# Optimization experiments

Hardware: AMD Instinct MI355X
Metric: run time of the kernel (lower is better)

## Reference

```python
import jax, jax.numpy as jnp
import numpy as np

L = 2
S = (L + 1) ** 2            # 9 spherical harmonic coefficients
C = 128                     # sphere_channels
H = 128                     # hidden_channels
NH = 8                      # num_heads
A = 32                      # attn_alpha_channels
V = 16                      # attn_value_channels
N = 5000                    # nodes
E = 50000                   # edges
DE = 128                    # invariant edge embedding dim
G = 18                      # S2 grid points

# l of each coefficient in l-major layout [S]
L_OF = np.concatenate([np.full(2 * l + 1, l) for l in range(L + 1)])
IDX_M0 = np.array([l * l + l for l in range(L + 1)])

def _idx_m(m):
    neg = np.array([l * l + l - m for l in range(m, L + 1)])
    pos = np.array([l * l + l + m for l in range(m, L + 1)])
    return neg, pos

IDX_M1_NEG, IDX_M1_POS = _idx_m(1)
IDX_M2_NEG, IDX_M2_POS = _idx_m(2)
# m-major ordering and its inverse permutation back to l-major
PERM = np.concatenate([IDX_M0, IDX_M1_POS, IDX_M1_NEG, IDX_M2_POS, IDX_M2_NEG])
INV_PERM = np.argsort(PERM)


def _silu(x):
    return x * jax.nn.sigmoid(x)


def _layernorm(x, g, b, eps=1e-5):
    mu = x.mean(-1, keepdims=True)
    var = ((x - mu) ** 2).mean(-1, keepdims=True)
    return (x - mu) * jax.lax.rsqrt(var + eps) * g + b


def _smooth_leaky_relu(x, a=0.2):
    return 0.5 * (1 + a) * x + 0.5 * (1 - a) * x * (2 * jax.nn.sigmoid(x) - 1)


def _so2_conv(x, w_m0, b_m0, w_m1, w_m2, cout):
    """SO(2) convolution on rotated embeddings. x: [E,S,Cin] l-major.
    Returns ([E,S,cout] l-major, extra m=0 channels)."""
    e = x.shape[0]
    # m = 0: plain linear over flattened (L+1)*Cin
    x0 = x[:, IDX_M0, :].reshape(e, -1)
    y0 = x0 @ w_m0 + b_m0
    y0_main = y0[:, : (L + 1) * cout].reshape(e, L + 1, cout)
    y0_extra = y0[:, (L + 1) * cout:]
    parts = [y0_main]
    # m > 0: complex (cos/sin) SO2 mixing with shared weight for real/imag
    for neg, pos, w in ((IDX_M1_NEG, IDX_M1_POS, w_m1), (IDX_M2_NEG, IDX_M2_POS, w_m2)):
        nl = len(neg)
        xr = x[:, pos, :].reshape(e, -1)
        xi = x[:, neg, :].reshape(e, -1)
        yr = xr @ w  # [E, 2*nl*cout]
        yi = xi @ w
        yr_r, yr_i = yr[:, : nl * cout], yr[:, nl * cout:]
        yi_r, yi_i = yi[:, : nl * cout], yi[:, nl * cout:]
        parts.append((yr_r - yi_i).reshape(e, nl, cout))   # +m (real)
        parts.append((yr_i + yi_r).reshape(e, nl, cout))   # -m (imag)
    out_m = jnp.concatenate(parts, axis=1)                 # m-major
    return out_m[:, INV_PERM, :], y0_extra


def _s2_act(x, togrid, fromgrid):
    g = jnp.einsum('gs,esc->egc', togrid, x)
    return jnp.einsum('sg,egc->esc', fromgrid, _silu(g))


def _sep_s2_act(scalars, x, togrid, fromgrid):
    t = _s2_act(x, togrid, fromgrid)
    return jnp.concatenate([_silu(scalars)[:, None, :], t[:, 1:, :]], axis=1)


def _so3_linear(x, w, b):
    # w: [L+1, Cin, Cout], shared across m within each l; bias only on l=0
    out = jnp.einsum('nsc,sco->nso', x, w[L_OF])
    return out.at[:, 0, :].add(b)


def _eqv_norm(x, g, b, eps=1e-5):
    # l=0: layernorm over channels; l>0: RMS over (m, channels) per degree
    outs = [_layernorm(x[:, 0:1, :], g[0], b)]
    for l in range(1, L + 1):
        sl = x[:, l * l:(l + 1) * (l + 1), :]
        rms = jnp.sqrt(jnp.mean(sl ** 2, axis=(1, 2), keepdims=True) + eps)
        outs.append(sl / rms * g[l])
    return jnp.concatenate(outs, axis=1)


def _forward(x, edge_distance, wigner, rad_w1, rad_b1, rad_ln_g, rad_ln_b, rad_w2, rad_b2,
             w1_m0, b1_m0, w1_m1, w1_m2, w2_m0, b2_m0, w2_m1, w2_m2,
             alpha_ln_g, alpha_ln_b, alpha_dot, proj_w, proj_b,
             norm1_g, norm1_b, norm2_g, norm2_b,
             gate_w, gate_b, ffn_w1, ffn_b1, ffn_w2, ffn_b2,
             togrid, fromgrid, edge_src, edge_dst):
    # ---------- SO2 equivariant graph attention ----------
    xn = _eqv_norm(x, norm1_g, norm1_b)
    msg = jnp.concatenate([xn[edge_src], xn[edge_dst]], axis=-1)      # [E,S,2C]
    msg = jnp.einsum('eij,ejc->eic', wigner, msg)                     # rotate to edge frame
    # radial function shared across m within each l (use_m_share_rad)
    h = _silu(_layernorm(edge_distance @ rad_w1 + rad_b1, rad_ln_g, rad_ln_b))
    rad = (h @ rad_w2 + rad_b2).reshape(-1, L + 1, 2 * C)             # [E,L+1,2C]
    msg = msg * rad[:, L_OF, :]
    hid, x0_extra = _so2_conv(msg, w1_m0, b1_m0, w1_m1, w1_m2, H)
    x_alpha = x0_extra[:, : NH * A].reshape(-1, NH, A)
    gating = x0_extra[:, NH * A:]                                     # [E,H]
    hid = _sep_s2_act(gating, hid, togrid, fromgrid)
    val, _ = _so2_conv(hid, w2_m0, b2_m0, w2_m1, w2_m2, NH * V)
    val = jnp.einsum('eji,ejc->eic', wigner, val)                     # rotate back (D^T)
    # attention weights with per-destination segment softmax
    a = _smooth_leaky_relu(_layernorm(x_alpha, alpha_ln_g, alpha_ln_b))
    a = jnp.einsum('eha,ha->eh', a, alpha_dot)                        # [E,NH]
    amax = jax.ops.segment_max(a, edge_dst, num_segments=N)
    aexp = jnp.exp(a - amax[edge_dst])
    asum = jax.ops.segment_sum(aexp, edge_dst, num_segments=N)
    attn = aexp / asum[edge_dst]
    msg_out = (val.reshape(-1, S, NH, V) * attn[:, None, :, None]).reshape(-1, S, NH * V)
    node = jax.ops.segment_sum(msg_out, edge_dst, num_segments=N)     # [N,S,NH*V]
    x = x + _so3_linear(node, proj_w, proj_b)
    # ---------- spherical FFN (sep S2 gating) ----------
    xn = _eqv_norm(x, norm2_g, norm2_b)
    gating = xn[:, 0, :] @ gate_w + gate_b
    hh = _so3_linear(xn, ffn_w1, ffn_b1)
    hh = _sep_s2_act(gating, hh, togrid, fromgrid)
    return x + _so3_linear(hh, ffn_w2, ffn_b2)


def setup_inputs() -> dict:
    key = jax.random.key(0)
    ks = iter(jax.random.split(key, 64))
    def nrm(shape, scale=1.0):
        return jax.random.normal(next(ks), shape, dtype=jnp.float32) * scale
    EX = NH * A + H
    inp = {}
    inp['x'] = nrm((N, S, C))
    inp['edge_distance'] = nrm((E, DE))
    inp['wigner'] = nrm((E, S, S), 1.0 / np.sqrt(S))
    inp['rad_w1'] = nrm((DE, 64), 1.0 / np.sqrt(DE)); inp['rad_b1'] = jnp.zeros((64,), jnp.float32)
    inp['rad_ln_g'] = jnp.ones((64,), jnp.float32); inp['rad_ln_b'] = jnp.zeros((64,), jnp.float32)
    inp['rad_w2'] = nrm((64, 2 * C * (L + 1)), 0.05); inp['rad_b2'] = jnp.ones((2 * C * (L + 1),), jnp.float32)
    inp['w1_m0'] = nrm(((L + 1) * 2 * C, (L + 1) * H + EX), 1.0 / np.sqrt((L + 1) * 2 * C))
    inp['b1_m0'] = jnp.zeros(((L + 1) * H + EX,), jnp.float32)
    inp['w1_m1'] = nrm((2 * 2 * C, 2 * 2 * H), 1.0 / np.sqrt(2 * 2 * C))
    inp['w1_m2'] = nrm((2 * C, 2 * H), 1.0 / np.sqrt(2 * C))
    inp['w2_m0'] = nrm(((L + 1) * H, (L + 1) * NH * V), 1.0 / np.sqrt((L + 1) * H))
    inp['b2_m0'] = jnp.zeros(((L + 1) * NH * V,), jnp.float32)
    inp['w2_m1'] = nrm((2 * H, 2 * 2 * NH * V), 1.0 / np.sqrt(2 * H))
    inp['w2_m2'] = nrm((H, 2 * NH * V), 1.0 / np.sqrt(H))
    inp['alpha_ln_g'] = jnp.ones((A,), jnp.float32); inp['alpha_ln_b'] = jnp.zeros((A,), jnp.float32)
    inp['alpha_dot'] = nrm((NH, A), 1.0 / np.sqrt(A))
    inp['proj_w'] = nrm((L + 1, NH * V, C), 1.0 / np.sqrt(NH * V)); inp['proj_b'] = jnp.zeros((C,), jnp.float32)
    inp['norm1_g'] = jnp.ones((L + 1, C), jnp.float32); inp['norm1_b'] = jnp.zeros((C,), jnp.float32)
    inp['norm2_g'] = jnp.ones((L + 1, C), jnp.float32); inp['norm2_b'] = jnp.zeros((C,), jnp.float32)
    inp['gate_w'] = nrm((C, H), 1.0 / np.sqrt(C)); inp['gate_b'] = jnp.zeros((H,), jnp.float32)
    inp['ffn_w1'] = nrm((L + 1, C, H), 1.0 / np.sqrt(C)); inp['ffn_b1'] = jnp.zeros((H,), jnp.float32)
    inp['ffn_w2'] = nrm((L + 1, H, C), 1.0 / np.sqrt(H)); inp['ffn_b2'] = jnp.zeros((C,), jnp.float32)
    inp['togrid'] = nrm((G, S), 1.0 / np.sqrt(S))
    inp['fromgrid'] = nrm((S, G), 1.0 / np.sqrt(G))
    inp['edge_src'] = jax.random.randint(next(ks), (E,), 0, N)
    inp['edge_dst'] = jax.random.randint(next(ks), (E,), 0, N)
    return inp


def reference(x, edge_distance, wigner, rad_w1, rad_b1, rad_ln_g, rad_ln_b, rad_w2, rad_b2,
              w1_m0, b1_m0, w1_m1, w1_m2, w2_m0, b2_m0, w2_m1, w2_m2,
              alpha_ln_g, alpha_ln_b, alpha_dot, proj_w, proj_b,
              norm1_g, norm1_b, norm2_g, norm2_b,
              gate_w, gate_b, ffn_w1, ffn_b1, ffn_w2, ffn_b2,
              togrid, fromgrid, edge_src, edge_dst):
    return _forward(x, edge_distance, wigner, rad_w1, rad_b1, rad_ln_g, rad_ln_b, rad_w2, rad_b2,
                    w1_m0, b1_m0, w1_m1, w1_m2, w2_m0, b2_m0, w2_m1, w2_m2,
                    alpha_ln_g, alpha_ln_b, alpha_dot, proj_w, proj_b,
                    norm1_g, norm1_b, norm2_g, norm2_b,
                    gate_w, gate_b, ffn_w1, ffn_b1, ffn_w2, ffn_b2,
                    togrid, fromgrid, edge_src, edge_dst)
```

## Files before the change

kernel.cpp:

```cpp
#include <hip/hip_runtime.h>
#include <hip/hip_bf16.h>

typedef unsigned short u16;
typedef unsigned int   u32;
typedef __attribute__((ext_vector_type(8))) short short8;
typedef __attribute__((ext_vector_type(4))) float float4v;

#define NN 5000
#define EE 50000

__device__ __forceinline__ float b2f(u16 u){ return __uint_as_float(((u32)u)<<16); }
__device__ __forceinline__ u16 f2b(float f){
  u32 x = __float_as_uint(f);
  u32 r = (x + 0x7fffu + ((x>>16)&1u)) >> 16;
  return (u16)r;
}
__device__ __forceinline__ float ldin(const void* p, size_t i, bool f32){
  return f32 ? ((const float*)p)[i] : b2f(((const u16*)p)[i]);
}
__device__ __forceinline__ float siluf(float x){ return x/(1.f+__expf(-x)); }
__device__ __forceinline__ float waveRedSum(float v){
  #pragma unroll
  for (int m=32;m>=1;m>>=1) v += __shfl_xor(v,m,64);
  return v;
}
__device__ __forceinline__ float red32(float v){
  #pragma unroll
  for (int m=16;m>=1;m>>=1) v += __shfl_xor(v,m,64);
  return v;
}


__global__ __launch_bounds__(256) void zero_kernel(float* __restrict__ p, int n){
  for (int i = blockIdx.x*256 + threadIdx.x; i < n; i += gridDim.x*256) p[i] = 0.f;
}

__global__ void detect_kernel(const u32* __restrict__ ng, int* __restrict__ flag){
  if (blockIdx.x == 0 && threadIdx.x == 0) *flag = (ng[0] == 0x3F800000u) ? 1 : 0;
}

__global__ __launch_bounds__(256) void hist_kernel(const int* __restrict__ edst,
    int* __restrict__ counts){
  int e = blockIdx.x*256 + threadIdx.x;
  if (e < EE) atomicAdd(&counts[edst[e]], 1);
}

__global__ __launch_bounds__(1024) void scan_kernel(const int* __restrict__ counts,
    int* __restrict__ row_start, int* __restrict__ cursor){
  __shared__ int buf[1024];
  __shared__ int base;
  const int t = threadIdx.x;
  if (t == 0){ base = 0; row_start[0] = 0; }
  __syncthreads();
  for (int i0 = 0; i0 < NN; i0 += 1024){
    int i = i0 + t;
    int c = (i < NN) ? counts[i] : 0;
    buf[t] = c;
    __syncthreads();
    #pragma unroll
    for (int ofs = 1; ofs < 1024; ofs <<= 1){
      int v = (t >= ofs) ? buf[t-ofs] : 0;
      __syncthreads();
      buf[t] += v;
      __syncthreads();
    }
    if (i < NN){
      int incl = base + buf[t];
      row_start[i+1] = incl;
      cursor[i] = incl - c;
    }
    __syncthreads();
    if (t == 0) base += buf[1023];
    __syncthreads();
  }
}

__global__ __launch_bounds__(256) void place_kernel(const int* __restrict__ edst,
    int* __restrict__ cursor, int* __restrict__ order){
  int e = blockIdx.x*256 + threadIdx.x;
  if (e < EE) order[atomicAdd(&cursor[edst[e]], 1)] = e;
}

__global__ __launch_bounds__(256) void cvt_kernel(const int* __restrict__ dflag,
    const void* __restrict__ src, long long off0, u16* __restrict__ dst, int n){
  const bool f32 = (*dflag != 0);
  for (int i = blockIdx.x*256 + threadIdx.x; i < n; i += gridDim.x*256)
    dst[i] = f32 ? f2b(((const float*)src)[off0 + i]) : ((const u16*)src)[off0 + i];
}

__global__ __launch_bounds__(256) void gathercvt_kernel(const int* __restrict__ dflag,
    const void* __restrict__ src, const int* __restrict__ order, int e0,
    u16* __restrict__ dst, int n){
  const bool f32 = (*dflag != 0);
  for (int i = blockIdx.x*256 + threadIdx.x; i < n; i += gridDim.x*256){
    int le = i >> 7, c = i & 127;
    int eg = order[e0 + le];
    dst[i] = f2b(ldin(src, (size_t)eg*128 + c, f32));
  }
}

__global__ __launch_bounds__(256) void biasprep_kernel(const int* __restrict__ dflag,
    const void* b1,const void* b2,const void* rb1,const void* rb2,
    const void* pb,const void* gb,const void* f1,const void* f2,
    u16* d_b1,u16* d_b2,u16* d_rb1,u16* d_rb2,u16* d_pb,u16* d_gb,u16* d_f1,u16* d_f2){
  const bool f32 = (*dflag != 0);
  int t = blockIdx.x*256 + threadIdx.x;
  if (t < 768) d_b1[t]  = f2b(ldin(b1, t, f32));
  if (t < 384) d_b2[t]  = f2b(ldin(b2, t, f32));
  if (t < 64)  d_rb1[t] = f2b(ldin(rb1, t, f32));
  if (t < 768) d_rb2[t] = f2b(ldin(rb2, t, f32));
  if (t < 128){
    d_pb[t] = f2b(ldin(pb, t, f32));
    d_gb[t] = f2b(ldin(gb, t, f32));
    d_f1[t] = f2b(ldin(f1, t, f32));
    d_f2[t] = f2b(ldin(f2, t, f32));
  }
}

__global__ __launch_bounds__(256) void cvtT_kernel(const int* __restrict__ dflag,
    const void* __restrict__ src, long long off0, u16* __restrict__ dst, int K, int N){
  const bool f32 = (*dflag != 0);
  int total = K*N;
  for (int i = blockIdx.x*256 + threadIdx.x; i < total; i += gridDim.x*256){
    int n = i / K, k = i % K;
    dst[i] = f2b(ldin(src, (size_t)off0 + (size_t)k*N + n, f32));
  }
}

__global__ __launch_bounds__(256) void cvtT3_kernel(const int* __restrict__ dflag,
    const void* __restrict__ src, u16* __restrict__ dst){
  const bool f32 = (*dflag != 0);
  const long long l = blockIdx.y;
  for (int i = blockIdx.x*256 + threadIdx.x; i < 16384; i += gridDim.x*256){
    int n = i >> 7, k = i & 127;
    dst[l*16384 + i] = f2b(ldin(src, (size_t)l*16384 + (size_t)k*128 + n, f32));
  }
}

__global__ __launch_bounds__(256) void wprepT_kernel(const int* __restrict__ dflag,
    const void* __restrict__ w, u16* __restrict__ wt, int K0, int N0){
  const bool f32 = (*dflag != 0);
  int total = 2*N0*2*K0;
  for (int i = blockIdx.x*blockDim.x + threadIdx.x; i < total; i += gridDim.x*blockDim.x){
    int c = i / (2*K0), r = i % (2*K0);
    float v;
    if (r < K0) v = ldin(w, (size_t)r*2*N0 + c, f32);
    else {
      int rr = r - K0;
      if (c < N0) v = -ldin(w, (size_t)rr*2*N0 + N0 + c, f32);
      else        v =  ldin(w, (size_t)rr*2*N0 + (c - N0), f32);
    }
    wt[i] = f2b(v);
  }
}

__global__ __launch_bounds__(128) void eqvnorm_kernel(const int* __restrict__ dflag,
    const void* __restrict__ x, int in_always_f32,
    const void* __restrict__ g, const void* __restrict__ b,
    void* __restrict__ out, int out_f32){
  const bool f32 = (*dflag != 0);
  const bool inf32 = in_always_f32 || f32;
  const int n = blockIdx.x, t = threadIdx.x;
  __shared__ float red[2];
  float v[9];
  #pragma unroll
  for (int s=0;s<9;s++) v[s] = ldin(x, (size_t)n*1152 + s*128 + t, inf32);

  auto bsum = [&](float val)->float{
    float w = waveRedSum(val);
    __syncthreads();
    if ((t & 63) == 0) red[t>>6] = w;
    __syncthreads();
    return red[0] + red[1];
  };
  auto store = [&](int idx, float val){
    if (out_f32) ((float*)out)[(size_t)n*1152 + idx] = val;
    else         ((u16*) out)[(size_t)n*1152 + idx] = f2b(val);
  };
  float mu  = bsum(v[0]) * (1.f/128.f);
  float d0  = v[0] - mu;
  float var = bsum(d0*d0) * (1.f/128.f);
  store(t, d0 * rsqrtf(var + 1e-5f) * ldin(g, t, f32) + ldin(b, t, f32));
  float ss1 = v[1]*v[1] + v[2]*v[2] + v[3]*v[3];
  float inv1 = rsqrtf(bsum(ss1)*(1.f/384.f) + 1e-5f);
  float g1 = ldin(g, 128 + t, f32);
  #pragma unroll
  for (int s=1;s<=3;s++) store(s*128 + t, v[s]*inv1*g1);
  float ss2 = 0.f;
  #pragma unroll
  for (int s=4;s<9;s++) ss2 += v[s]*v[s];
  float inv2 = rsqrtf(bsum(ss2)*(1.f/640.f) + 1e-5f);
  float g2 = ldin(g, 256 + t, f32);
  #pragma unroll
  for (int s=4;s<9;s++) store(s*128 + t, v[s]*inv2*g2);
}

__global__ __launch_bounds__(256) void gemm_mfma_kernel(
    const u16* __restrict__ A, int lda, int K,
    const u16* __restrict__ Wt, int NOUT,
    const u16* __restrict__ bias,
    u16* __restrict__ out0, int ld0, int coloff0, int split,
    u16* __restrict__ out1, int ld1, int M){
  __shared__ __align__(16) u16 As[2][128][40];
  __shared__ __align__(16) u16 Bs[2][128][40];
  const int t = threadIdx.x;
  const int r0 = blockIdx.x * 128;
  const int n0 = blockIdx.y * 128;
  const int lane = t & 63, wave = t >> 6;
  const int wr = (wave & 1) * 64, wn = (wave >> 1) * 64;
  float4v acc[4][4];
  #pragma unroll
  for (int i=0;i<4;i++)
    #pragma unroll
    for (int j=0;j<4;j++) acc[i][j] = (float4v){0.f,0.f,0.f,0.f};

  const int sr = t >> 2, sc = (t & 3) * 8;
  const int fr = lane & 15, fq = (lane >> 4) * 8;

  const u16* aptr0 = A + (size_t)(r0 + sr)*lda + sc;
  const u16* aptr1 = A + (size_t)(r0 + sr + 64)*lda + sc;
  const bool av0 = (r0 + sr) < M, av1 = (r0 + sr + 64) < M;
  const u16* bptr0 = Wt + (size_t)(n0 + sr)*K + sc;
  const u16* bptr1 = Wt + (size_t)(n0 + sr + 64)*K + sc;
  const bool bv0 = (n0 + sr) < NOUT, bv1 = (n0 + sr + 64) < NOUT;
  const uint4 z4 = make_uint4(0u,0u,0u,0u);

  uint4 ra0 = av0 ? *(const uint4*)(aptr0) : z4;
  uint4 ra1 = av1 ? *(const uint4*)(aptr1) : z4;
  uint4 rb0 = bv0 ? *(const uint4*)(bptr0) : z4;
  uint4 rb1 = bv1 ? *(const uint4*)(bptr1) : z4;

  int buf = 0;
  for (int k0 = 0; k0 < K; k0 += 32){
    *(uint4*)&As[buf][sr   ][sc] = ra0;
    *(uint4*)&As[buf][sr+64][sc] = ra1;
    *(uint4*)&Bs[buf][sr   ][sc] = rb0;
    *(uint4*)&Bs[buf][sr+64][sc] = rb1;
    __syncthreads();
    const int k1 = k0 + 32;
    if (k1 < K){
      ra0 = av0 ? *(const uint4*)(aptr0 + k1) : z4;
      ra1 = av1 ? *(const uint4*)(aptr1 + k1) : z4;
      rb0 = bv0 ? *(const uint4*)(bptr0 + k1) : z4;
      rb1 = bv1 ? *(const uint4*)(bptr1 + k1) : z4;
    }
    short8 af[4], bfv[4];
    #pragma unroll
    for (int i=0;i<4;i++){
      af[i]  = *(const short8*)&As[buf][wr + i*16 + fr][fq];
      bfv[i] = *(const short8*)&Bs[buf][wn + i*16 + fr][fq];
    }
    #pragma unroll
    for (int i=0;i<4;i++)
      #pragma unroll
      for (int j=0;j<4;j++)
        acc[i][j] = __builtin_amdgcn_mfma_f32_16x16x32_bf16(af[i], bfv[j], acc[i][j], 0, 0, 0);
    buf ^= 1;
    __syncthreads();
  }
  const int quad = lane >> 4;
  #pragma unroll
  for (int j=0;j<4;j++){
    int col = n0 + wn + j*16 + fr;
    if (col >= NOUT) continue;
    float bv = bias ? b2f(bias[col]) : 0.f;
    #pragma unroll
    for (int i=0;i<4;i++){
      int rbase = r0 + wr + i*16 + quad*4;
      #pragma unroll
      for (int rg=0; rg<4; rg++){
        int row = rbase + rg;
        if (row >= M) continue;
        float v = acc[i][j][rg] + bv;
        if (col < split) out0[(size_t)row*ld0 + coloff0 + col] = f2b(v);
        else             out1[(size_t)row*ld1 + (col - split)] = f2b(v);
      }
    }
  }
}

__global__ __launch_bounds__(256) void gemm_node_kernel(
    const int* __restrict__ dflag,
    const u16* __restrict__ A,
    const u16* __restrict__ W3t,
    const u16* __restrict__ bias,
    const void* __restrict__ resid, int resid_mode,
    void* __restrict__ out, int out_mode, int gate_out){
  const bool f32 = (*dflag != 0);
  const int l = blockIdx.y;
  const int rpn  = (l==0) ? 1 : ((l==1) ? 3 : 5);
  const int soff = (l==0) ? 0 : ((l==1) ? 1 : 4);
  const int M = NN * rpn;
  const int r0 = blockIdx.x * 128;
  if (r0 >= M) return;
  __shared__ __align__(16) u16 As[128][40];
  __shared__ __align__(16) u16 Bs[128][40];
  const int t = threadIdx.x;
  const int lane = t & 63, wave = t >> 6;
  const int wr = (wave & 1) * 64, wn = (wave >> 1) * 64;
  float4v acc[4][4];
  #pragma unroll
  for (int i=0;i<4;i++)
    #pragma unroll
    for (int j=0;j<4;j++) acc[i][j] = (float4v){0.f,0.f,0.f,0.f};

  const int sr = t >> 2, sc = (t & 3) * 8;
  const int fr = lane & 15, fq = (lane >> 4) * 8;
  size_t abase[2]; bool aval[2];
  #pragma unroll
  for (int s2=0;s2<2;s2++){
    int m = r0 + sr + s2*64;
    aval[s2] = m < M;
    int n = m / rpn, srow = soff + (m % rpn);
    abase[s2] = (size_t)n*1152 + srow*128 + sc;
  }
  const u16* Wl = W3t + (size_t)l*16384;

  #pragma unroll
  for (int k0 = 0; k0 < 128; k0 += 32){
    #pragma unroll
    for (int s2=0;s2<2;s2++){
      int row = sr + s2*64;
      uint4 av = make_uint4(0u,0u,0u,0u);
      if (aval[s2]) av = *(const uint4*)(A + abase[s2] + k0);
      *(uint4*)&As[row][sc] = av;
      uint4 wv = *(const uint4*)(Wl + (size_t)row*128 + k0 + sc);
      *(uint4*)&Bs[row][sc] = wv;
    }
    __syncthreads();
    short8 af[4], bfr[4];
    #pragma unroll
    for (int i=0;i<4;i++){
      af[i]  = *(const short8*)&As[wr + i*16 + fr][fq];
      bfr[i] = *(const short8*)&Bs[wn + i*16 + fr][fq];
    }
    #pragma unroll
    for (int i=0;i<4;i++)
      #pragma unroll
      for (int j=0;j<4;j++)
        acc[i][j] = __builtin_amdgcn_mfma_f32_16x16x32_bf16(af[i], bfr[j], acc[i][j], 0, 0, 0);
    __syncthreads();
  }
  const int quad = lane >> 4;
  #pragma unroll
  for (int j=0;j<4;j++){
    int col = wn + j*16 + fr;
    float bv = (bias && l==0) ? b2f(bias[col]) : 0.f;
    #pragma unroll
    for (int i=0;i<4;i++){
      int rbase = r0 + wr + i*16 + quad*4;
      #pragma unroll
      for (int rg=0; rg<4; rg++){
        int m = rbase + rg;
        if (m >= M) continue;
        int n = m / rpn, srow = soff + (m % rpn);
        size_t na = (size_t)n*1152 + srow*128 + col;
        float v = acc[i][j][rg] + bv;
        if (resid_mode == 1)      v += ((const float*)resid)[na];
        else if (resid_mode == 2) v += ldin(resid, na, f32);
        if (gate_out)            ((u16*)out)[(size_t)n*128 + col] = f2b(v);
        else if (out_mode == 0)  ((u16*)out)[na] = f2b(v);
        else if (out_mode == 1)  ((float*)out)[na] = v;
        else { if (f32) ((float*)out)[na] = v; else ((u16*)out)[na] = f2b(v); }
      }
    }
  }
}

__global__ __launch_bounds__(256) void nodecvt_kernel(const float* __restrict__ node,
    const float* __restrict__ nsum, u16* __restrict__ nodeb){
  for (int i = blockIdx.x*256 + threadIdx.x; i < NN*1152; i += gridDim.x*256){
    int n = i / 1152, c = i & 127, h = c >> 4;
    float ns = nsum[(size_t)n*8 + h];
    float rs = (ns > 0.f) ? 1.f/ns : 0.f;
    nodeb[i] = f2b(node[i] * rs);
  }
}

__global__ __launch_bounds__(128) void node_s2act_kernel(const int* __restrict__ dflag,
    const u16* __restrict__ hh, const u16* __restrict__ gating,
    const void* __restrict__ tg, const void* __restrict__ fg, u16* __restrict__ hh2){
  const bool f32 = (*dflag != 0);
  const int n = blockIdx.x, t = threadIdx.x;
  __shared__ float TG[162], FG[162];
  for (int i=t; i<162; i+=128){ TG[i]=ldin(tg,i,f32); FG[i]=ldin(fg,i,f32); }
  float hv[9];
  #pragma unroll
  for (int s=0;s<9;s++) hv[s] = b2f(hh[(size_t)n*1152 + s*128 + t]);
  __syncthreads();
  float gg[18];
  #pragma unroll
  for (int gi=0;gi<18;gi++){
    float a = 0.f;
    #pragma unroll
    for (int s=0;s<9;s++) a = fmaf(TG[gi*9+s], hv[s], a);
    gg[gi] = siluf(a);
  }
  hh2[(size_t)n*1152 + t] = f2b(siluf(b2f(gating[(size_t)n*128 + t])));
  #pragma unroll
  for (int s=1;s<9;s++){
    float a = 0.f;
    #pragma unroll
    for (int gi=0;gi<18;gi++) a = fmaf(FG[s*18+gi], gg[gi], a);
    hh2[(size_t)n*1152 + s*128 + t] = f2b(a);
  }
}

__global__ __launch_bounds__(256) void lnsilu_kernel(const int* __restrict__ dflag,
    u16* __restrict__ H, const void* __restrict__ rlng, const void* __restrict__ rlnb, int M){
  const bool f32 = (*dflag != 0);
  const int r = blockIdx.x*4 + (threadIdx.x >> 6), lane = threadIdx.x & 63;
  if (r >= M) return;
  float h = b2f(H[(size_t)r*64 + lane]);
  float mu = waveRedSum(h) * (1.f/64.f);
  float d = h - mu;
  float var = waveRedSum(d*d) * (1.f/64.f);
  float hn = d * rsqrtf(var + 1e-5f) * ldin(rlng, lane, f32) + ldin(rlnb, lane, f32);
  H[(size_t)r*64 + lane] = f2b(siluf(hn));
}

__global__ __launch_bounds__(256) void edge_rot_kernel(const int* __restrict__ dflag,
    const u16* __restrict__ xn, const void* __restrict__ wig,
    const u16* __restrict__ rad,
    const int* __restrict__ esrc, const int* __restrict__ edst,
    const int* __restrict__ order, int e0, u16* __restrict__ msg){
  const bool f32 = (*dflag != 0);
  const int le = blockIdx.x, t = threadIdx.x;
  const int eg = order[e0 + le];
  __shared__ float W[81];
  if (t < 81) W[t] = ldin(wig, (size_t)eg*81 + t, f32);
  const int src = esrc[eg], dst = edst[eg];
  float pre[9];
  const u16* base = (t < 128) ? (xn + (size_t)src*1152 + t) : (xn + (size_t)dst*1152 + (t-128));
  #pragma unroll
  for (int j=0;j<9;j++) pre[j] = b2f(base[j*128]);
  __syncthreads();
  float rot[9];
  #pragma unroll
  for (int i=0;i<9;i++){
    float a = 0.f;
    #pragma unroll
    for (int j=0;j<9;j++) a = fmaf(W[i*9+j], pre[j], a);
    rot[i] = a;
  }
  float r[3];
  #pragma unroll
  for (int l=0;l<3;l++) r[l] = b2f(rad[(size_t)le*768 + l*256 + t]);
  const int INVP[9] = {0,5,1,3,8,6,2,4,7};
  const int LOF[9]  = {0,1,1,1,2,2,2,2,2};
  u16* mb = msg + (size_t)le*2304 + t;
  #pragma unroll
  for (int i=0;i<9;i++) mb[INVP[i]*256] = f2b(rot[i] * r[LOF[i]]);
}

__global__ __launch_bounds__(256) void s2act_alpha_kernel(const int* __restrict__ dflag,
    const u16* __restrict__ hid, const u16* __restrict__ extra,
    const void* __restrict__ togrid, const void* __restrict__ fromgrid,
    const void* __restrict__ alng, const void* __restrict__ alnb, const void* __restrict__ adot,
    const int* __restrict__ edst, const int* __restrict__ order, int e0,
    u16* __restrict__ hid2, float* __restrict__ aexp, float* __restrict__ nsum){
  const bool f32 = (*dflag != 0);
  const int le = blockIdx.x, t = threadIdx.x;
  const int p = e0 + le;
  __shared__ float TG[162], FG[162];
  if (t < 162){ TG[t] = ldin(togrid, t, f32); FG[t] = ldin(fromgrid, t, f32); }
  {
    const int h = t >> 5, ai = t & 31;
    float v = b2f(extra[(size_t)le*384 + t]);
    float mu = red32(v) * (1.f/32.f);
    float d = v - mu;
    float var = red32(d*d) * (1.f/32.f);
    float xh = d * rsqrtf(var + 1e-5f) * ldin(alng, ai, f32) + ldin(alnb, ai, f32);
    float sig = 1.f/(1.f + __expf(-xh));
    float sl = 0.6f*xh + 0.4f*xh*(2.f*sig - 1.f);
    float pp = sl * ldin(adot, h*32 + ai, f32);
    float dot = red32(pp);
    if (ai == 0){
      float ex = __expf(dot - 8.f);
      aexp[(size_t)p*8 + h] = ex;
      atomicAdd(&nsum[(size_t)edst[order[p]]*8 + h], ex);
    }
  }
  __syncthreads();
  if (t < 128){
    const int INVP[9] = {0,5,1,3,8,6,2,4,7};
    float hv[9];
    #pragma unroll
    for (int s=0;s<9;s++) hv[s] = b2f(hid[(size_t)le*1152 + INVP[s]*128 + t]);
    float gg[18];
    #pragma unroll
    for (int gi=0;gi<18;gi++){
      float a = 0.f;
      #pragma unroll
      for (int s=0;s<9;s++) a = fmaf(TG[gi*9+s], hv[s], a);
      gg[gi] = siluf(a);
    }
    hid2[(size_t)le*1152 + t] = f2b(siluf(b2f(extra[(size_t)le*384 + 256 + t])));
    #pragma unroll
    for (int s=1;s<9;s++){
      float a = 0.f;
      #pragma unroll
      for (int gi=0;gi<18;gi++) a = fmaf(FG[s*18+gi], gg[gi], a);
      hid2[(size_t)le*1152 + INVP[s]*128 + t] = f2b(a);
    }
  }
}

__global__ __launch_bounds__(128) void unrot_gather_kernel(const int* __restrict__ dflag,
    const u16* __restrict__ val, const void* __restrict__ wig,
    const float* __restrict__ aexp, const int* __restrict__ order,
    const int* __restrict__ row_start, int e0, int Mc, float* __restrict__ node){
  const bool f32 = (*dflag != 0);
  const int n = blockIdx.x, t = threadIdx.x;
  const int s = row_start[n], tend = row_start[n+1];
  int lo = (s > e0) ? s : e0;
  int hi = (tend < e0 + Mc) ? tend : (e0 + Mc);
  if (lo >= hi) return;
  __shared__ float W[81];
  __shared__ float SC[8];
  const int INVP[9] = {0,5,1,3,8,6,2,4,7};
  float acc[9];
  #pragma unroll
  for (int i=0;i<9;i++) acc[i] = 0.f;
  for (int p = lo; p < hi; p++){
    const int le = p - e0;
    const int eg = order[p];
    __syncthreads();
    if (t < 81) W[t] = ldin(wig, (size_t)eg*81 + t, f32);
    if (t >= 120) SC[t-120] = aexp[(size_t)p*8 + (t-120)];
    __syncthreads();
    float vs[9];
    #pragma unroll
    for (int j=0;j<9;j++) vs[j] = b2f(val[(size_t)le*1152 + INVP[j]*128 + t]);
    const float sc = SC[t>>4];
    #pragma unroll
    for (int i=0;i<9;i++){
      float a = 0.f;
      #pragma unroll
      for (int j=0;j<9;j++) a = fmaf(W[j*9+i], vs[j], a);
      acc[i] = fmaf(a, sc, acc[i]);
    }
  }
  const bool full = (s >= e0) && (tend <= e0 + Mc);
  #pragma unroll
  for (int i=0;i<9;i++){
    float* dst = &node[(size_t)n*1152 + i*128 + t];
    if (full) *dst = acc[i];
    else      atomicAdd(dst, acc[i]);
  }
}

extern "C" void kernel_launch(void* const* d_in, const int* in_sizes, int n_in,
                              void* d_out, int out_size, void* d_ws, size_t ws_size,
                              hipStream_t stream){
  (void)in_sizes; (void)n_in; (void)out_size;
  const void* x       = d_in[0];
  const void* edist   = d_in[1];
  const void* wig     = d_in[2];
  const void* rad_w1  = d_in[3];
  const void* rad_b1  = d_in[4];
  const void* rad_lng = d_in[5];
  const void* rad_lnb = d_in[6];
  const void* rad_w2  = d_in[7];
  const void* rad_b2  = d_in[8];
  const void* w1_m0   = d_in[9];
  const void* b1_m0   = d_in[10];
  const void* w1_m1   = d_in[11];
  const void* w1_m2   = d_in[12];
  const void* w2_m0   = d_in[13];
  const void* b2_m0   = d_in[14];
  const void* w2_m1   = d_in[15];
  const void* w2_m2   = d_in[16];
  const void* alng    = d_in[17];
  const void* alnb    = d_in[18];
  const void* adot    = d_in[19];
  const void* proj_w  = d_in[20];
  const void* proj_b  = d_in[21];
  const void* norm1_g = d_in[22];
  const void* norm1_b = d_in[23];
  const void* norm2_g = d_in[24];
  const void* norm2_b = d_in[25];
  const void* gate_w  = d_in[26];
  const void* gate_b  = d_in[27];
  const void* ffn_w1  = d_in[28];
  const void* ffn_b1  = d_in[29];
  const void* ffn_w2  = d_in[30];
  const void* ffn_b2  = d_in[31];
  const void* togrid  = d_in[32];
  const void* fromgrid= d_in[33];
  const int* esrc     = (const int*)d_in[34];
  const int* edst     = (const int*)d_in[35];

  char* wsp = (char*)d_ws;
  size_t off = 0;
  auto alloc = [&](size_t bytes)->char*{
    char* p = wsp + off;
    off = (off + bytes + 255) & ~(size_t)255;
    return p;
  };
  int*  dflag  = (int*) alloc(4);
  u16*  W1cT   = (u16*) alloc((size_t)512*1024*2);
  u16*  W2cT   = (u16*) alloc((size_t)256*512*2);
  u16*  W3cT   = (u16*) alloc((size_t)512*512*2);
  u16*  W4cT   = (u16*) alloc((size_t)256*256*2);
  u16*  w1m0T  = (u16*) alloc((size_t)768*768*2);
  u16*  b1m0C  = (u16*) alloc((size_t)768*2);
  u16*  w2m0T  = (u16*) alloc((size_t)384*384*2);
  u16*  b2m0C  = (u16*) alloc((size_t)384*2);
  u16*  rw1T   = (u16*) alloc((size_t)64*128*2);
  u16*  rb1C   = (u16*) alloc((size_t)64*2);
  u16*  rw2T   = (u16*) alloc((size_t)768*64*2);
  u16*  rb2C   = (u16*) alloc((size_t)768*2);
  u16*  projT3 = (u16*) alloc((size_t)3*16384*2);
  u16*  ffn1T3 = (u16*) alloc((size_t)3*16384*2);
  u16*  ffn2T3 = (u16*) alloc((size_t)3*16384*2);
  u16*  gateT  = (u16*) alloc((size_t)16384*2);
  u16*  pbC    = (u16*) alloc((size_t)128*2);
  u16*  gbC    = (u16*) alloc((size_t)128*2);
  u16*  fb1C   = (u16*) alloc((size_t)128*2);
  u16*  fb2C   = (u16*) alloc((size_t)128*2);
  u16*  xn     = (u16*) alloc((size_t)NN*1152*2);
  float* aexp  = (float*)alloc((size_t)EE*8*4);
  float* nsum  = (float*)alloc((size_t)NN*8*4);
  float* node  = (float*)alloc((size_t)NN*1152*4);
  int*  counts = (int*) alloc((size_t)NN*4);
  int*  row_st = (int*) alloc((size_t)(NN+1)*4);
  int*  cursor = (int*) alloc((size_t)NN*4);
  int*  order  = (int*) alloc((size_t)EE*4);
  size_t fixed_end = off;
  size_t avail = (ws_size > fixed_end) ? (ws_size - fixed_end) : 0;

  long long cap = ((long long)avail - 4096) / 7680;
  int Ec;
  if (cap >= 50048) Ec = 50048;
  else {
    long long c128 = cap & ~127LL;
    if (c128 < 128) c128 = 128;
    int nch = (EE + (int)c128 - 1) / (int)c128;
    Ec = ((EE + nch - 1) / nch + 127) & ~127;
  }
  char* cb = wsp + fixed_end;
  u16* msgC   = (u16*)cb;
  u16* hidC   = (u16*)(cb + (size_t)Ec*2304*2);
  u16* extraC = (u16*)(cb + (size_t)Ec*2304*2 + (size_t)Ec*1152*2);
  u16* hid2C  = msgC;
  u16* valC   = hidC;
  u16* edistC = msgC;
  u16* radC   = hidC;
  u16* HrawC  = hidC + (size_t)Ec*768;
  u16*  nodeb  = (u16*)cb;
  float* xnew  = (float*)(cb + (size_t)NN*1152*2);
  u16*  xn2    = (u16*)(cb + (size_t)NN*1152*2 + (size_t)NN*1152*4);
  u16*  gating = xn2 + (size_t)NN*1152;
  u16*  hh     = gating + (size_t)NN*128;
  u16*  hh2    = hh + (size_t)NN*1152;

  detect_kernel<<<1, 64, 0, stream>>>((const u32*)norm1_g, dflag);

  zero_kernel<<<2048, 256, 0, stream>>>(nsum, NN*8 + NN*1152 + NN);

  hist_kernel<<<(EE+255)/256, 256, 0, stream>>>(edst, counts);
  scan_kernel<<<1, 1024, 0, stream>>>(counts, row_st, cursor);
  place_kernel<<<(EE+255)/256, 256, 0, stream>>>(edst, cursor, order);

  cvtT_kernel<<<2304, 256, 0, stream>>>(dflag, w1_m0, 0, w1m0T, 768, 768);
  cvtT_kernel<<<576,  256, 0, stream>>>(dflag, w2_m0, 0, w2m0T, 384, 384);
  cvtT_kernel<<<32,   256, 0, stream>>>(dflag, rad_w1, 0, rw1T, 128, 64);
  cvtT_kernel<<<192,  256, 0, stream>>>(dflag, rad_w2, 0, rw2T, 64, 768);
  cvtT3_kernel<<<dim3(64,3), 256, 0, stream>>>(dflag, proj_w, projT3);
  cvtT3_kernel<<<dim3(64,3), 256, 0, stream>>>(dflag, ffn_w1, ffn1T3);
  cvtT3_kernel<<<dim3(64,3), 256, 0, stream>>>(dflag, ffn_w2, ffn2T3);
  cvtT_kernel<<<64, 256, 0, stream>>>(dflag, gate_w, 0, gateT, 128, 128);
  biasprep_kernel<<<3, 256, 0, stream>>>(dflag, b1_m0, b2_m0, rad_b1, rad_b2,
                                         proj_b, gate_b, ffn_b1, ffn_b2,
                                         b1m0C, b2m0C, rb1C, rb2C, pbC, gbC, fb1C, fb2C);
  wprepT_kernel<<<2048, 256, 0, stream>>>(dflag, w1_m1, W1cT, 512, 256);
  wprepT_kernel<<<512,  256, 0, stream>>>(dflag, w1_m2, W2cT, 256, 128);
  wprepT_kernel<<<1024, 256, 0, stream>>>(dflag, w2_m1, W3cT, 256, 256);
  wprepT_kernel<<<256,  256, 0, stream>>>(dflag, w2_m2, W4cT, 128, 128);

  eqvnorm_kernel<<<NN, 128, 0, stream>>>(dflag, x, 0, norm1_g, norm1_b, xn, 0);

  for (int e0 = 0; e0 < EE; e0 += Ec){
    int Mc = (EE - e0 < Ec) ? (EE - e0) : Ec;
    int GX = (Mc + 127) / 128;
    gathercvt_kernel<<<dim3((Mc*128+255)/256), 256, 0, stream>>>(dflag, edist, order, e0,
                                                                 edistC, Mc*128);
    gemm_mfma_kernel<<<dim3(GX,1), 256, 0, stream>>>(edistC, 128, 128, rw1T, 64, rb1C,
                                                     HrawC, 64, 0, 64, nullptr, 0, Mc);
    lnsilu_kernel<<<dim3((Mc+3)/4), 256, 0, stream>>>(dflag, HrawC, rad_lng, rad_lnb, Mc);
    gemm_mfma_kernel<<<dim3(GX,6), 256, 0, stream>>>(HrawC, 64, 64, rw2T, 768, rb2C,
                                                     radC, 768, 0, 768, nullptr, 0, Mc);
    edge_rot_kernel<<<Mc, 256, 0, stream>>>(dflag, xn, wig, radC, esrc, edst, order, e0, msgC);
    gemm_mfma_kernel<<<dim3(GX,6), 256, 0, stream>>>(msgC,        2304, 768,  w1m0T, 768, b1m0C,
                                                     hidC, 1152, 0,   384, extraC, 384, Mc);
    gemm_mfma_kernel<<<dim3(GX,4), 256, 0, stream>>>(msgC + 768,  2304, 1024, W1cT,  512, nullptr,
                                                     hidC, 1152, 384, 512, nullptr, 0, Mc);
    gemm_mfma_kernel<<<dim3(GX,2), 256, 0, stream>>>(msgC + 1792, 2304, 512,  W2cT,  256, nullptr,
                                                     hidC, 1152, 896, 256, nullptr, 0, Mc);
    s2act_alpha_kernel<<<Mc, 256, 0, stream>>>(dflag, hidC, extraC, togrid, fromgrid, alng,
                                               alnb, adot, edst, order, e0, hid2C, aexp, nsum);
    gemm_mfma_kernel<<<dim3(GX,3), 256, 0, stream>>>(hid2C,       1152, 384, w2m0T, 384, b2m0C,
                                                     valC, 1152, 0,   384, nullptr, 0, Mc);
    gemm_mfma_kernel<<<dim3(GX,4), 256, 0, stream>>>(hid2C + 384, 1152, 512, W3cT,  512, nullptr,
                                                     valC, 1152, 384, 512, nullptr, 0, Mc);
    gemm_mfma_kernel<<<dim3(GX,2), 256, 0, stream>>>(hid2C + 896, 1152, 256, W4cT,  256, nullptr,
                                                     valC, 1152, 896, 256, nullptr, 0, Mc);
    unrot_gather_kernel<<<NN, 128, 0, stream>>>(dflag, valC, wig, aexp, order, row_st,
                                                e0, Mc, node);
  }

  const int GN2 = (NN*5 + 127)/128;
  nodecvt_kernel<<<2048, 256, 0, stream>>>(node, nsum, nodeb);
  gemm_node_kernel<<<dim3(GN2,3), 256, 0, stream>>>(dflag, nodeb, projT3, pbC,
                                                    x, 2, xnew, 1, 0);
  eqvnorm_kernel<<<NN, 128, 0, stream>>>(dflag, xnew, 1, norm2_g, norm2_b, xn2, 0);
  gemm_node_kernel<<<dim3((NN+127)/128,1), 256, 0, stream>>>(dflag, xn2, gateT, gbC,
                                                             nullptr, 0, gating, 0, 1);
  gemm_node_kernel<<<dim3(GN2,3), 256, 0, stream>>>(dflag, xn2, ffn1T3, fb1C,
                                                    nullptr, 0, hh, 0, 0);
  node_s2act_kernel<<<NN, 128, 0, stream>>>(dflag, hh, gating, togrid, fromgrid, hh2);
  gemm_node_kernel<<<dim3(GN2,3), 256, 0, stream>>>(dflag, hh2, ffn2T3, fb2C,
                                                    xnew, 1, d_out, 2, 0);
}
```

Measured before the change: 1.216 ms.

## Load GEMM tiles directly into LDS via global_load_lds with double buffering

Replaces the register-staged global-to-LDS copy in the MFMA GEMM with direct global_load_lds (16-byte) writes into an unpadded LDS tile. The next tile's load is issued before the current tile's MFMAs, and there is one barrier per iteration. This removes the VGPR round-trip and the LDS store instructions. The LDS padding is dropped, so fragment reads may hit bank conflicts. Rows that fail the bounds check are no longer zero-filled, so stale LDS data could feed the MFMAs for partial tiles. There is also no explicit vmcnt wait before the barrier, which could be a correctness risk.

```diff
diff --git a/kernel.cpp b/kernel.cpp
--- a/kernel.cpp
+++ b/kernel.cpp
@@ -28,6 +28,10 @@
   #pragma unroll
   for (int m=16;m>=1;m>>=1) v += __shfl_xor(v,m,64);
   return v;
+}
+__device__ __forceinline__ void gload_lds16(const u16* g, u16* l){
+  __builtin_amdgcn_global_load_lds((const __attribute__((address_space(1))) void*)g,
+                                   (__attribute__((address_space(3))) void*)l, 16, 0, 0);
 }
 
 
@@ -201,8 +205,8 @@
     const u16* __restrict__ bias,
     u16* __restrict__ out0, int ld0, int coloff0, int split,
     u16* __restrict__ out1, int ld1, int M){
-  __shared__ __align__(16) u16 As[2][128][40];
-  __shared__ __align__(16) u16 Bs[2][128][40];
+  __shared__ __align__(16) u16 As[2][128*32];
+  __shared__ __align__(16) u16 Bs[2][128*32];
   const int t = threadIdx.x;
   const int r0 = blockIdx.x * 128;
   const int n0 = blockIdx.y * 128;
@@ -214,49 +218,48 @@
     #pragma unroll
     for (int j=0;j<4;j++) acc[i][j] = (float4v){0.f,0.f,0.f,0.f};
 
-  const int sr = t >> 2, sc = (t & 3) * 8;
   const int fr = lane & 15, fq = (lane >> 4) * 8;
 
-  const u16* aptr0 = A + (size_t)(r0 + sr)*lda + sc;
-  const u16* aptr1 = A + (size_t)(r0 + sr + 64)*lda + sc;
-  const bool av0 = (r0 + sr) < M, av1 = (r0 + sr + 64) < M;
-  const u16* bptr0 = Wt + (size_t)(n0 + sr)*K + sc;
-  const u16* bptr1 = Wt + (size_t)(n0 + sr + 64)*K + sc;
-  const bool bv0 = (n0 + sr) < NOUT, bv1 = (n0 + sr + 64) < NOUT;
-  const uint4 z4 = make_uint4(0u,0u,0u,0u);
-
-  uint4 ra0 = av0 ? *(const uint4*)(aptr0) : z4;
-  uint4 ra1 = av1 ? *(const uint4*)(aptr1) : z4;
-  uint4 rb0 = bv0 ? *(const uint4*)(bptr0) : z4;
-  uint4 rb1 = bv1 ? *(const uint4*)(bptr1) : z4;
-
-  int buf = 0;
+  const int Rw   = wave * 32;
+  const int srow = lane >> 2;
+  const int scol = (lane & 3) * 8;
+  const u16* aG0 = A  + (size_t)(r0 + Rw + srow) * lda + scol;
+  const u16* aG1 = aG0 + (size_t)16 * lda;
+  const bool aV0 = (r0 + Rw + srow)      < M;
+  const bool aV1 = (r0 + Rw + 16 + srow) < M;
+  const u16* bG0 = Wt + (size_t)(n0 + Rw + srow) * K + scol;
+  const u16* bG1 = bG0 + (size_t)16 * K;
+  const bool bV0 = (n0 + Rw + srow)      < NOUT;
+  const bool bV1 = (n0 + Rw + 16 + srow) < NOUT;
+
+  auto stage = [&](int buf, int k0){
+    u16* lA = &As[buf][Rw * 32];
+    u16* lB = &Bs[buf][Rw * 32];
+    if (aV0) gload_lds16(aG0 + k0, lA);
+    if (aV1) gload_lds16(aG1 + k0, lA + 16*32);
+    if (bV0) gload_lds16(bG0 + k0, lB);
+    if (bV1) gload_lds16(bG1 + k0, lB + 16*32);
+  };
+
+  stage(0, 0);
+  __syncthreads();
+  int cur = 0;
   for (int k0 = 0; k0 < K; k0 += 32){
-    *(uint4*)&As[buf][sr   ][sc] = ra0;
-    *(uint4*)&As[buf][sr+64][sc] = ra1;
-    *(uint4*)&Bs[buf][sr   ][sc] = rb0;
-    *(uint4*)&Bs[buf][sr+64][sc] = rb1;
-    __syncthreads();
     const int k1 = k0 + 32;
-    if (k1 < K){
-      ra0 = av0 ? *(const uint4*)(aptr0 + k1) : z4;
-      ra1 = av1 ? *(const uint4*)(aptr1 + k1) : z4;
-      rb0 = bv0 ? *(const uint4*)(bptr0 + k1) : z4;
-      rb1 = bv1 ? *(const uint4*)(bptr1 + k1) : z4;
-    }
+    if (k1 < K) stage(cur ^ 1, k1);
     short8 af[4], bfv[4];
     #pragma unroll
     for (int i=0;i<4;i++){
-      af[i]  = *(const short8*)&As[buf][wr + i*16 + fr][fq];
-      bfv[i] = *(const short8*)&Bs[buf][wn + i*16 + fr][fq];
+      af[i]  = *(const short8*)&As[cur][(wr + i*16 + fr)*32 + fq];
+      bfv[i] = *(const short8*)&Bs[cur][(wn + i*16 + fr)*32 + fq];
     }
     #pragma unroll
     for (int i=0;i<4;i++)
       #pragma unroll
       for (int j=0;j<4;j++)
         acc[i][j] = __builtin_amdgcn_mfma_f32_16x16x32_bf16(af[i], bfv[j], acc[i][j], 0, 0, 0);
-    buf ^= 1;
-    __syncthreads();
+    __syncthreads();
+    cur ^= 1;
   }
   const int quad = lane >> 4;
   #pragma unroll
```

Measured after the change: 1.227 ms. No clear change (+0.9%).
